# Kernel optimization log

Hardware: AMD Instinct MI355X
Metric: run time of the kernel (lower is better)

The kernel has to match this reference:

```python
import jax, jax.numpy as jnp
import numpy as np

N_ATOMS = 100000
N_BONDS = 200000
N_MOLS = 4000
ATOMS_PER_MOL = 25
MAX_NB = 6
ATOM_FDIM = 133
BOND_FDIM = 14
HIDDEN = 300
DEPTH = 3


def setup_inputs() -> dict:
    key = jax.random.key(0)
    ks = jax.random.split(key, 8)
    f_atoms = jax.random.normal(ks[0], (N_ATOMS, ATOM_FDIM), dtype=jnp.float32)
    f_bonds = jax.random.normal(ks[1], (N_BONDS, BOND_FDIM), dtype=jnp.float32)
    # incoming-bond lists per atom (irregular gather targets)
    a2b = jax.random.randint(ks[2], (N_ATOMS, MAX_NB), 0, N_BONDS, dtype=jnp.int32)
    # source atom of each directed bond
    b2a = jax.random.randint(ks[3], (N_BONDS,), 0, N_ATOMS, dtype=jnp.int32)
    # reverse bond: directed bonds come in pairs (2i, 2i+1)
    b2revb = (jnp.arange(N_BONDS, dtype=jnp.int32) ^ 1)
    # contiguous [start, size] per molecule
    starts = jnp.arange(N_MOLS, dtype=jnp.int32) * ATOMS_PER_MOL
    sizes = jnp.full((N_MOLS,), ATOMS_PER_MOL, dtype=jnp.int32)
    a_scope = jnp.stack([starts, sizes], axis=1)
    W_i = jax.random.normal(ks[4], (HIDDEN, ATOM_FDIM + BOND_FDIM), dtype=jnp.float32) * 0.05
    W_h = jax.random.normal(ks[5], (HIDDEN, HIDDEN), dtype=jnp.float32) * 0.05
    W_o = jax.random.normal(ks[6], (HIDDEN, ATOM_FDIM + HIDDEN), dtype=jnp.float32) * 0.05
    b_o = jax.random.normal(ks[7], (HIDDEN,), dtype=jnp.float32) * 0.05
    return {"f_atoms": f_atoms, "f_bonds": f_bonds, "a2b": a2b, "b2a": b2a,
            "b2revb": b2revb, "a_scope": a_scope, "W_i": W_i, "W_h": W_h,
            "W_o": W_o, "b_o": b_o}


def reference(f_atoms, f_bonds, a2b, b2a, b2revb, a_scope, W_i, W_h, W_o, b_o):
    # initial directed-bond messages: [f_atoms[src], f_bonds] -> Linear -> ReLU
    input_feats = jnp.concatenate([f_atoms[b2a], f_bonds], axis=1)  # (E, 147)
    message = jax.nn.relu(input_feats @ W_i.T)  # (E, H)
    for _ in range(DEPTH - 1):
        nei_a_message = message[a2b].sum(axis=1)          # (V, H) gather+sum
        nei_message = nei_a_message[b2a] - message[b2revb]  # (E, H)
        message = jax.nn.relu(nei_message @ W_h.T)
    a_message = message[a2b].sum(axis=1)  # (V, H)
    atom_hiddens = jax.nn.relu(jnp.concatenate([f_atoms, a_message], axis=1) @ W_o.T + b_o)
    # vectorized scope mean-pool (scopes are contiguous ranges)
    starts = a_scope[:, 0]
    sizes = a_scope[:, 1]
    seg_ids = jnp.searchsorted(starts, jnp.arange(atom_hiddens.shape[0]), side='right') - 1
    sums = jax.ops.segment_sum(atom_hiddens, seg_ids, num_segments=N_MOLS)
    denom = jnp.maximum(sizes, 1).astype(atom_hiddens.dtype)[:, None]
    mol_vecs = jnp.where((sizes > 0)[:, None], sums / denom, 0.0)
    return mol_vecs
```

## Files before the change

kernel.cpp:

```cpp
#include <hip/hip_runtime.h>
#include <stdint.h>

#define N_ATOMS   100000
#define N_BONDS   200000
#define N_MOLS    4000
#define MAX_NB    6
#define ATOM_FDIM 133
#define BOND_FDIM 14
#define HIDDEN    300
#define NPAD      320

typedef __attribute__((ext_vector_type(8))) short          bf16x8;
typedef __attribute__((ext_vector_type(8))) unsigned short u16x8;
typedef __attribute__((ext_vector_type(4))) float          f32x4;
typedef __attribute__((ext_vector_type(4))) unsigned int   u32x4;

static __device__ __forceinline__ float u2f(unsigned int u) {
  union { unsigned int u; float f; } v; v.u = u; return v.f;
}
static __device__ __forceinline__ unsigned int f2u(float f) {
  union { float f; unsigned int u; } v; v.f = f; return v.u;
}
static __device__ __forceinline__ float bflo(unsigned int u) { return u2f(u << 16); }
static __device__ __forceinline__ float bfhi(unsigned int u) { return u2f(u & 0xffff0000u); }
static __device__ __forceinline__ unsigned short f2bf_rn(float f) {
  unsigned int u = f2u(f);
  return (unsigned short)((u + 0x7fffu + ((u >> 16) & 1u)) >> 16);
}
static __device__ __forceinline__ unsigned int pack_rn(float lo, float hi) {
  return ((unsigned int)f2bf_rn(hi) << 16) | f2bf_rn(lo);
}

__global__ __launch_bounds__(256) void convin_kernel(
    const float* __restrict__ w, unsigned short* __restrict__ o, int N, int K, int KP) {
  size_t total = (size_t)N * KP;
  for (size_t idx = (size_t)blockIdx.x * 256 + threadIdx.x; idx < total; idx += (size_t)gridDim.x * 256) {
    int n = (int)(idx / KP), k = (int)(idx - (size_t)n * KP);
    float v = (k < K) ? w[(size_t)n * K + k] : 0.f;
    o[idx] = f2bf_rn(v);
  }
}

__global__ __launch_bounds__(256) void convw_kernel(
    const float* __restrict__ w, unsigned short* __restrict__ o,
    int Ksrc, int seg1, int src2off, int seg2dst, int seg2len, int KP) {
  int total = NPAD * KP;
  for (int idx = blockIdx.x * 256 + threadIdx.x; idx < total; idx += gridDim.x * 256) {
    int n = idx / KP, k = idx - n * KP;
    int src = -1;
    if (k < seg1) src = k;
    else if (k >= seg2dst && k < seg2dst + seg2len) src = src2off + (k - seg2dst);
    float v = (n < HIDDEN && src >= 0) ? w[(size_t)n * Ksrc + src] : 0.f;
    o[idx] = f2bf_rn(v);
  }
}

template<int KP, int SEG, bool RELU>
__global__ __launch_bounds__(256) void gemm_tp(
    const unsigned short* S1, const unsigned short* __restrict__ S2,
    const int* __restrict__ gmap, const unsigned short* __restrict__ W,
    unsigned short* out, int M, int nTiles) {
  constexpr int CHUNKS = KP / 8;
  constexpr int NST    = KP / 32;
  __shared__ __align__(16) unsigned short As[2 * 64 * KP];

  const int tid  = threadIdx.x;
  const int lane = tid & 63;
  const int wv   = tid >> 6;
  const int ar   = lane & 15, kq = lane >> 4;
  const int nbase = wv * 80;
  const unsigned short* Wl = W + (size_t)(nbase + ar) * KP + kq * 8;

  auto rowof = [&](int tile) { int r = tile * 64 + lane; return (r < M) ? r : (M - 1); };

  auto stage = [&](int buf, int drow, int srow) {
    char* base = (char*)As + (size_t)buf * (64 * KP * 2);
#pragma unroll
    for (int cs = wv; cs < CHUNKS; cs += 4) {
      const unsigned short* src;
      if (SEG == 0) src = S1 + (size_t)drow * KP + cs * 8;
      else src = (cs < 20) ? (S1 + (size_t)srow * 160 + cs * 8)
                           : (S2 + (size_t)drow * 32 + (cs - 20) * 8);
      __builtin_amdgcn_global_load_lds(
          (const __attribute__((address_space(1))) void*)src,
          (__attribute__((address_space(3))) void*)(base + (size_t)cs * 1024), 16, 0, 0);
    }
  };

  f32x4 acc[4][5];

  auto compute = [&](int buf) {
    const char* base = (const char*)As + (size_t)buf * (64 * KP * 2);
    bf16x8 bnxt[5];
#pragma unroll
    for (int nf = 0; nf < 5; nf++) bnxt[nf] = *(const bf16x8*)(Wl + (size_t)nf * 16 * KP);
#pragma unroll
    for (int ks = 0; ks < NST; ks++) {
      bf16x8 bcur[5];
#pragma unroll
      for (int nf = 0; nf < 5; nf++) bcur[nf] = bnxt[nf];
      if (ks + 1 < NST) {
#pragma unroll
        for (int nf = 0; nf < 5; nf++)
          bnxt[nf] = *(const bf16x8*)(Wl + (size_t)nf * 16 * KP + (ks + 1) * 32);
      }
      bf16x8 af[4];
#pragma unroll
      for (int m = 0; m < 4; m++)
        af[m] = *(const bf16x8*)(base + (size_t)((ks * 4 + kq) * 64 + m * 16 + ar) * 16);
#pragma unroll
      for (int nf = 0; nf < 5; nf++)
#pragma unroll
        for (int m = 0; m < 4; m++)
          acc[m][nf] = __builtin_amdgcn_mfma_f32_16x16x32_bf16(af[m], bcur[nf], acc[m][nf], 0, 0, 0);
    }
  };

  auto storeC = [&](int tile) {
#pragma unroll
    for (int m = 0; m < 4; m++)
#pragma unroll
      for (int rr = 0; rr < 4; rr++) {
        int orow = tile * 64 + m * 16 + kq * 4 + rr;
        if (orow >= M) continue;
#pragma unroll
        for (int nf = 0; nf < 5; nf++) {
          float v = acc[m][nf][rr];
          if (RELU) v = v > 0.f ? v : 0.f;
          out[(size_t)orow * NPAD + nbase + nf * 16 + ar] = f2bf_rn(v);
        }
      }
  };

  int t = blockIdx.x;
  if (t >= nTiles) return;
  {
    int srow0 = (SEG == 1) ? gmap[rowof(t)] : 0;
    stage(0, rowof(t), srow0);
  }
  int tn = t + gridDim.x;
  int g_n = (SEG == 1 && tn < nTiles) ? gmap[rowof(tn)] : 0;
  __syncthreads();

  int cur = 0;
  while (t < nTiles) {
    const int nxt = t + gridDim.x;
    if (nxt < nTiles) stage(cur ^ 1, rowof(nxt), g_n);
    const int t2 = nxt + gridDim.x;
    int g_n2 = (SEG == 1 && t2 < nTiles) ? gmap[rowof(t2)] : 0;
#pragma unroll
    for (int m = 0; m < 4; m++)
#pragma unroll
      for (int n = 0; n < 5; n++) acc[m][n] = (f32x4){0.f, 0.f, 0.f, 0.f};
    compute(cur);
    __syncthreads();
    storeC(t);
    cur ^= 1; t = nxt; g_n = g_n2;
  }
}

__global__ __launch_bounds__(256) void gemm_tpf(
    const unsigned short* Z, const unsigned short* __restrict__ Nei,
    const int* __restrict__ b2a, const unsigned short* __restrict__ W,
    unsigned short* out, int nTiles) {
  constexpr int KP = 320, NST = 10, NREG = 10;
  __shared__ __align__(16) unsigned short As[2 * 64 * KP];

  const int tid  = threadIdx.x;
  const int lane = tid & 63;
  const int wv   = tid >> 6;
  const int ar   = lane & 15, kq = lane >> 4;
  const int nbase = wv * 80;
  const unsigned short* Wl = W + (size_t)(nbase + ar) * KP + kq * 8;

  u32x4 nei4[NREG], z4[NREG];

  auto loadreg = [&](int tile) {
    const int row = tile * 64 + lane;
    const int g   = b2a[row];
    const int rev = row ^ 1;
#pragma unroll
    for (int i = 0; i < NREG; i++) {
      const int cs = i * 4 + wv;
      nei4[i] = *(const u32x4*)(Nei + (size_t)g * NPAD + cs * 8);
      z4[i]   = *(const u32x4*)(Z + (size_t)rev * NPAD + cs * 8);
    }
  };

  auto writestage = [&](int buf) {
    char* base = (char*)As + (size_t)buf * (64 * KP * 2);
#pragma unroll
    for (int i = 0; i < NREG; i++) {
      const int cs = i * 4 + wv;
      u32x4 o;
#pragma unroll
      for (int t4 = 0; t4 < 4; t4++) {
        float lo = bflo(nei4[i][t4]) - bflo(z4[i][t4]);
        float hi = bfhi(nei4[i][t4]) - bfhi(z4[i][t4]);
        lo = lo > 0.f ? lo : 0.f; hi = hi > 0.f ? hi : 0.f;
        o[t4] = pack_rn(lo, hi);
      }
      *(u32x4*)(base + (size_t)(cs * 64 + lane) * 16) = o;
    }
  };

  f32x4 acc[4][5];

  auto compute = [&](int buf) {
    const char* base = (const char*)As + (size_t)buf * (64 * KP * 2);
#pragma unroll
    for (int ks = 0; ks < NST; ks++) {
      bf16x8 af[4];
#pragma unroll
      for (int m = 0; m < 4; m++)
        af[m] = *(const bf16x8*)(base + (size_t)((ks * 4 + kq) * 64 + m * 16 + ar) * 16);
#pragma unroll
      for (int nf = 0; nf < 5; nf++) {
        bf16x8 bfr = *(const bf16x8*)(Wl + (size_t)nf * 16 * KP + ks * 32);
#pragma unroll
        for (int m = 0; m < 4; m++)
          acc[m][nf] = __builtin_amdgcn_mfma_f32_16x16x32_bf16(af[m], bfr, acc[m][nf], 0, 0, 0);
      }
    }
  };

  auto storeC = [&](int tile) {
#pragma unroll
    for (int m = 0; m < 4; m++)
#pragma unroll
      for (int rr = 0; rr < 4; rr++) {
        int orow = tile * 64 + m * 16 + kq * 4 + rr;
#pragma unroll
        for (int nf = 0; nf < 5; nf++)
          out[(size_t)orow * NPAD + nbase + nf * 16 + ar] = f2bf_rn(acc[m][nf][rr]);
      }
  };

  int t = blockIdx.x;
  if (t >= nTiles) return;
  loadreg(t);
  writestage(0);
  __syncthreads();

  int cur = 0;
  while (t < nTiles) {
    const int nxt = t + gridDim.x;
    if (nxt < nTiles) loadreg(nxt);
#pragma unroll
    for (int m = 0; m < 4; m++)
#pragma unroll
      for (int n = 0; n < 5; n++) acc[m][n] = (f32x4){0.f, 0.f, 0.f, 0.f};
    compute(cur);
    if (nxt < nTiles) writestage(cur ^ 1);
    __syncthreads();
    storeC(t);
    cur ^= 1; t = nxt;
  }
}

__global__ __launch_bounds__(256, 2) void gemm_bpo(
    const float* __restrict__ Af, const unsigned short* Ab,
    const unsigned short* __restrict__ W, const float* __restrict__ bias,
    unsigned short* out, int M) {
  constexpr int KP = 480, NST = 15;
  __shared__ __align__(16) unsigned short As[NST * 2048];

  const int b0   = blockIdx.x * 64;
  const int tid  = threadIdx.x;
  const int lane = tid & 63;
  const int wave = tid >> 6;
  const int sr   = tid >> 2;
  const int q    = tid & 3;

  int row = b0 + sr;
  if (row >= M) row = M - 1;
  const int dbase = (sr >> 4) * 512 + (q * 16 + (sr & 15)) * 8;

  auto stage_chunk = [&](int ks) -> u16x8 {
    const int kc = ks * 32 + q * 8;
    u16x8 r;
    if (kc >= 160) {
      r = *(const u16x8*)(Ab + (size_t)row * NPAD + (kc - 160));
    } else {
#pragma unroll
      for (int j = 0; j < 8; j++) {
        int k = kc + j;
        r[j] = (k < ATOM_FDIM) ? f2bf_rn(Af[(size_t)row * ATOM_FDIM + k]) : (unsigned short)0;
      }
    }
    return r;
  };

  constexpr int G = 5;
#pragma unroll
  for (int ks0 = 0; ks0 < NST; ks0 += G) {
    u16x8 vals[G];
#pragma unroll
    for (int j = 0; j < G; j++) { int ks = ks0 + j; if (ks < NST) vals[j] = stage_chunk(ks); }
#pragma unroll
    for (int j = 0; j < G; j++) { int ks = ks0 + j; if (ks < NST) *(u16x8*)&As[ks * 2048 + dbase] = vals[j]; }
  }
  __syncthreads();

  f32x4 acc[4][5];
#pragma unroll
  for (int m = 0; m < 4; m++)
#pragma unroll
    for (int n = 0; n < 5; n++) acc[m][n] = (f32x4){0.f, 0.f, 0.f, 0.f};

  const int nbase = wave * 80;
  const int ar = lane & 15, kq = lane >> 4;
  const unsigned short* Wl = W + (size_t)(nbase + ar) * KP + kq * 8;

  bf16x8 bnxt[5];
#pragma unroll
  for (int nf = 0; nf < 5; nf++) bnxt[nf] = *(const bf16x8*)(Wl + (size_t)nf * 16 * KP);

#pragma unroll
  for (int ks = 0; ks < NST; ks++) {
    bf16x8 bcur[5];
#pragma unroll
    for (int nf = 0; nf < 5; nf++) bcur[nf] = bnxt[nf];
    if (ks + 1 < NST) {
#pragma unroll
      for (int nf = 0; nf < 5; nf++)
        bnxt[nf] = *(const bf16x8*)(Wl + (size_t)nf * 16 * KP + (ks + 1) * 32);
    }
    bf16x8 af[4];
#pragma unroll
    for (int m = 0; m < 4; m++) af[m] = *(const bf16x8*)&As[ks * 2048 + m * 512 + lane * 8];
#pragma unroll
    for (int nf = 0; nf < 5; nf++)
#pragma unroll
      for (int m = 0; m < 4; m++)
        acc[m][nf] = __builtin_amdgcn_mfma_f32_16x16x32_bf16(af[m], bcur[nf], acc[m][nf], 0, 0, 0);
  }

#pragma unroll
  for (int m = 0; m < 4; m++) {
#pragma unroll
    for (int rr = 0; rr < 4; rr++) {
      int orow = b0 + m * 16 + kq * 4 + rr;
      if (orow >= M) continue;
#pragma unroll
      for (int nf = 0; nf < 5; nf++) {
        int ocol = nbase + nf * 16 + ar;
        float v = acc[m][nf][rr];
        v += (ocol < HIDDEN) ? bias[ocol] : 0.f;
        v = v > 0.f ? v : 0.f;
        out[(size_t)orow * NPAD + ocol] = f2bf_rn(v);
      }
    }
  }
}

__global__ __launch_bounds__(256) void agg_kernel(
    const unsigned short* __restrict__ src, const int* __restrict__ a2b,
    unsigned short* __restrict__ dst) {
  const int TPA = NPAD / 16;
  int idx = blockIdx.x * 256 + threadIdx.x;
  if (idx >= N_ATOMS * TPA) return;
  int a  = idx / TPA;
  int kc = (idx - a * TPA) * 16;
  int bidx[MAX_NB];
#pragma unroll
  for (int j = 0; j < MAX_NB; j++) bidx[j] = a2b[a * MAX_NB + j];
  float slo[8], shi[8];
#pragma unroll
  for (int t = 0; t < 8; t++) { slo[t] = 0.f; shi[t] = 0.f; }
#pragma unroll
  for (int j = 0; j < MAX_NB; j++) {
    const u32x4* p = (const u32x4*)(src + (size_t)bidx[j] * NPAD + kc);
    u32x4 v0 = p[0], v1 = p[1];
#pragma unroll
    for (int t = 0; t < 4; t++) {
      slo[t]     += bflo(v0[t]); shi[t]     += bfhi(v0[t]);
      slo[4 + t] += bflo(v1[t]); shi[4 + t] += bfhi(v1[t]);
    }
  }
  u32x4 o0, o1;
#pragma unroll
  for (int t = 0; t < 4; t++) { o0[t] = pack_rn(slo[t], shi[t]); o1[t] = pack_rn(slo[4 + t], shi[4 + t]); }
  u32x4* qp = (u32x4*)(dst + (size_t)a * NPAD + kc);
  qp[0] = o0; qp[1] = o1;
}

__global__ __launch_bounds__(256) void combineH_kernel(
    const unsigned short* __restrict__ neiZ, const unsigned short* Zh,
    const int* __restrict__ b2a, unsigned short* msg) {
  const int TPB = NPAD / 16;
  const int NPAIR = N_BONDS / 2;
  int idx = blockIdx.x * 256 + threadIdx.x;
  if (idx >= NPAIR * TPB) return;
  int p  = idx / TPB;
  int kc = (idx - p * TPB) * 16;
  int b0i = 2 * p, b1i = 2 * p + 1;
  int g0 = b2a[b0i], g1 = b2a[b1i];
  const u32x4* pn0 = (const u32x4*)(neiZ + (size_t)g0 * NPAD + kc);
  const u32x4* pn1 = (const u32x4*)(neiZ + (size_t)g1 * NPAD + kc);
  const u32x4* pz0 = (const u32x4*)(Zh + (size_t)b1i * NPAD + kc);
  const u32x4* pz1 = (const u32x4*)(Zh + (size_t)b0i * NPAD + kc);
  u32x4 n00 = pn0[0], n01 = pn0[1], n10 = pn1[0], n11 = pn1[1];
  u32x4 z00 = pz0[0], z01 = pz0[1], z10 = pz1[0], z11 = pz1[1];
  u32x4 o00, o01, o10, o11;
#pragma unroll
  for (int t = 0; t < 4; t++) {
    float a, c;
    a = bflo(n00[t]) - bflo(z00[t]); c = bfhi(n00[t]) - bfhi(z00[t]);
    o00[t] = pack_rn(a > 0.f ? a : 0.f, c > 0.f ? c : 0.f);
    a = bflo(n01[t]) - bflo(z01[t]); c = bfhi(n01[t]) - bfhi(z01[t]);
    o01[t] = pack_rn(a > 0.f ? a : 0.f, c > 0.f ? c : 0.f);
    a = bflo(n10[t]) - bflo(z10[t]); c = bfhi(n10[t]) - bfhi(z10[t]);
    o10[t] = pack_rn(a > 0.f ? a : 0.f, c > 0.f ? c : 0.f);
    a = bflo(n11[t]) - bflo(z11[t]); c = bfhi(n11[t]) - bfhi(z11[t]);
    o11[t] = pack_rn(a > 0.f ? a : 0.f, c > 0.f ? c : 0.f);
  }
  u32x4* q0 = (u32x4*)(msg + (size_t)b0i * NPAD + kc);
  u32x4* q1 = (u32x4*)(msg + (size_t)b1i * NPAD + kc);
  q0[0] = o00; q0[1] = o01; q1[0] = o10; q1[1] = o11;
}

__global__ __launch_bounds__(256) void readout_kernel(
    const unsigned short* __restrict__ hidden, const int* __restrict__ a_scope,
    float* __restrict__ out) {
  const int TPM = NPAD / 8;
  int idx = blockIdx.x * 256 + threadIdx.x;
  if (idx >= N_MOLS * TPM) return;
  int m = idx / TPM;
  int c = (idx - m * TPM) * 8;
  int start = a_scope[m * 2], size = a_scope[m * 2 + 1];
  float s[8];
#pragma unroll
  for (int t = 0; t < 8; t++) s[t] = 0.f;
  for (int i = 0; i < size; i++) {
    const u32x4 v = *(const u32x4*)(hidden + (size_t)(start + i) * NPAD + c);
#pragma unroll
    for (int t = 0; t < 4; t++) { s[2 * t] += bflo(v[t]); s[2 * t + 1] += bfhi(v[t]); }
  }
  float inv = (size > 0) ? 1.f / (float)size : 0.f;
#pragma unroll
  for (int t = 0; t < 8; t++) {
    int col = c + t;
    if (col < HIDDEN) out[(size_t)m * HIDDEN + col] = s[t] * inv;
  }
}

extern "C" void kernel_launch(void* const* d_in, const int* in_sizes, int n_in,
                              void* d_out, int out_size, void* d_ws, size_t ws_size,
                              hipStream_t stream) {
  const float* f_atoms = (const float*)d_in[0];
  const float* f_bonds = (const float*)d_in[1];
  const int*   a2b     = (const int*)d_in[2];
  const int*   b2a     = (const int*)d_in[3];
  const int*   a_scope = (const int*)d_in[5];
  const float* W_i     = (const float*)d_in[6];
  const float* W_h     = (const float*)d_in[7];
  const float* W_o     = (const float*)d_in[8];
  const float* b_o     = (const float*)d_in[9];
  float* out = (float*)d_out;

  char* ws = (char*)d_ws;
  size_t off = 0;
  auto alloc = [&](size_t bytes) { size_t o = off; off += (bytes + 255) & ~(size_t)255; return o; };
  unsigned short* P     = (unsigned short*)(ws + alloc((size_t)N_BONDS * NPAD * 2));
  unsigned short* R     = (unsigned short*)(ws + alloc((size_t)N_ATOMS * NPAD * 2));
  unsigned short* fa_bf = (unsigned short*)(ws + alloc((size_t)N_ATOMS * 160 * 2));
  unsigned short* fb_bf = (unsigned short*)(ws + alloc((size_t)N_BONDS * 32 * 2));
  unsigned short* WiAB  = (unsigned short*)(ws + alloc((size_t)NPAD * 192 * 2));
  unsigned short* Wh    = (unsigned short*)(ws + alloc((size_t)NPAD * 320 * 2));
  unsigned short* Wo    = (unsigned short*)(ws + alloc((size_t)NPAD * 480 * 2));

  convin_kernel<<<2048, 256, 0, stream>>>(f_atoms, fa_bf, N_ATOMS, ATOM_FDIM, 160);
  convin_kernel<<<2048, 256, 0, stream>>>(f_bonds, fb_bf, N_BONDS, BOND_FDIM, 32);
  convw_kernel<<<(NPAD * 192 + 255) / 256, 256, 0, stream>>>(W_i, WiAB, 147, 133, 133, 160, 14, 192);
  convw_kernel<<<(NPAD * 320 + 255) / 256, 256, 0, stream>>>(W_h, Wh, 300, 300, 0, 0, 0, 320);
  convw_kernel<<<(NPAD * 480 + 255) / 256, 256, 0, stream>>>(W_o, Wo, 433, 133, 133, 160, 300, 480);

  const int nTilesB = N_BONDS / 64;
  const int gridA = (N_ATOMS + 63) / 64;
  const int gagg = (N_ATOMS * (NPAD / 16) + 255) / 256;
  const int gpar = ((N_BONDS / 2) * (NPAD / 16) + 255) / 256;

  gemm_tp<192, 1, true><<<768, 256, 0, stream>>>(
      fa_bf, fb_bf, b2a, WiAB, P, N_BONDS, nTilesB);

  gemm_tp<320, 0, false><<<512, 256, 0, stream>>>(
      P, nullptr, nullptr, Wh, P, N_BONDS, nTilesB);
  agg_kernel<<<gagg, 256, 0, stream>>>(P, a2b, R);

  gemm_tpf<<<512, 256, 0, stream>>>(P, R, b2a, Wh, P, nTilesB);

  agg_kernel<<<gagg, 256, 0, stream>>>(P, a2b, R);
  combineH_kernel<<<gpar, 256, 0, stream>>>(R, P, b2a, P);

  agg_kernel<<<gagg, 256, 0, stream>>>(P, a2b, R);
  gemm_bpo<<<gridA, 256, 0, stream>>>(f_atoms, R, Wo, b_o, R, N_ATOMS);

  readout_kernel<<<(N_MOLS * (NPAD / 8) + 255) / 256, 256, 0, stream>>>(R, a_scope, out);
}
```

Before: 654.7 us.

## Split gemm_tpf K dimension into two pipelined chunks to halve LDS and registers

The fused gather-subtract-ReLU GEMM now stages its A operand in two K-chunks of 160 instead of the full 320. Each chunk is prefetched into registers while the previous one is computed, so register staging arrays and LDS use drop by half. This is meant to raise occupancy and reduce register pressure. The cost is an extra barrier per tile and shorter compute phases in which to hide the gather latency.

```diff
diff --git a/kernel.cpp b/kernel.cpp
--- a/kernel.cpp
+++ b/kernel.cpp
@@ -163,8 +163,8 @@
     const unsigned short* Z, const unsigned short* __restrict__ Nei,
     const int* __restrict__ b2a, const unsigned short* __restrict__ W,
     unsigned short* out, int nTiles) {
-  constexpr int KP = 320, NST = 10, NREG = 10;
-  __shared__ __align__(16) unsigned short As[2 * 64 * KP];
+  constexpr int KP = 320, BK = 160, NCH = 2, NSTC = 5, NREG = 5;
+  __shared__ __align__(16) unsigned short As[2 * 64 * BK];
 
   const int tid  = threadIdx.x;
   const int lane = tid & 63;
@@ -175,20 +175,21 @@
 
   u32x4 nei4[NREG], z4[NREG];
 
-  auto loadreg = [&](int tile) {
+  auto loadreg = [&](int tile, int chunk) {
     const int row = tile * 64 + lane;
     const int g   = b2a[row];
     const int rev = row ^ 1;
+    const int kb  = chunk * BK;
 #pragma unroll
     for (int i = 0; i < NREG; i++) {
       const int cs = i * 4 + wv;
-      nei4[i] = *(const u32x4*)(Nei + (size_t)g * NPAD + cs * 8);
-      z4[i]   = *(const u32x4*)(Z + (size_t)rev * NPAD + cs * 8);
+      nei4[i] = *(const u32x4*)(Nei + (size_t)g * NPAD + kb + cs * 8);
+      z4[i]   = *(const u32x4*)(Z + (size_t)rev * NPAD + kb + cs * 8);
     }
   };
 
   auto writestage = [&](int buf) {
-    char* base = (char*)As + (size_t)buf * (64 * KP * 2);
+    char* base = (char*)As + (size_t)buf * (64 * BK * 2);
 #pragma unroll
     for (int i = 0; i < NREG; i++) {
       const int cs = i * 4 + wv;
@@ -206,17 +207,18 @@
 
   f32x4 acc[4][5];
 
-  auto compute = [&](int buf) {
-    const char* base = (const char*)As + (size_t)buf * (64 * KP * 2);
-#pragma unroll
-    for (int ks = 0; ks < NST; ks++) {
+  auto compute = [&](int buf, int chunk) {
+    const char* base = (const char*)As + (size_t)buf * (64 * BK * 2);
+    const int kb = chunk * BK;
+#pragma unroll
+    for (int ks = 0; ks < NSTC; ks++) {
       bf16x8 af[4];
 #pragma unroll
       for (int m = 0; m < 4; m++)
         af[m] = *(const bf16x8*)(base + (size_t)((ks * 4 + kq) * 64 + m * 16 + ar) * 16);
 #pragma unroll
       for (int nf = 0; nf < 5; nf++) {
-        bf16x8 bfr = *(const bf16x8*)(Wl + (size_t)nf * 16 * KP + ks * 32);
+        bf16x8 bfr = *(const bf16x8*)(Wl + (size_t)nf * 16 * KP + kb + ks * 32);
 #pragma unroll
         for (int m = 0; m < 4; m++)
           acc[m][nf] = __builtin_amdgcn_mfma_f32_16x16x32_bf16(af[m], bfr, acc[m][nf], 0, 0, 0);
@@ -238,23 +240,29 @@
 
   int t = blockIdx.x;
   if (t >= nTiles) return;
-  loadreg(t);
+  loadreg(t, 0);
   writestage(0);
   __syncthreads();
 
   int cur = 0;
   while (t < nTiles) {
-    const int nxt = t + gridDim.x;
-    if (nxt < nTiles) loadreg(nxt);
 #pragma unroll
     for (int m = 0; m < 4; m++)
 #pragma unroll
       for (int n = 0; n < 5; n++) acc[m][n] = (f32x4){0.f, 0.f, 0.f, 0.f};
-    compute(cur);
-    if (nxt < nTiles) writestage(cur ^ 1);
-    __syncthreads();
+#pragma unroll
+    for (int c = 0; c < NCH; c++) {
+      int nt = t, nc = c + 1;
+      if (nc == NCH) { nt = t + gridDim.x; nc = 0; }
+      const bool valid = nt < nTiles;
+      if (valid) loadreg(nt, nc);
+      compute(cur, c);
+      if (valid) writestage(cur ^ 1);
+      __syncthreads();
+      cur ^= 1;
+    }
     storeC(t);
-    cur ^= 1; t = nxt;
+    t += gridDim.x;
   }
 }
 
```

After: 641.7 us. -2.0%, faster.
